# Kernel tuning notes

Hardware: AMD Instinct MI355X
Metric: run time of the kernel (lower is better)

The kernel has to match this reference:

```python
import jax, jax.numpy as jnp
import numpy as np

B, N, E, F, U = 4096, 32, 5, 64, 128

def setup_inputs() -> dict:
    key = jax.random.key(0)
    k1, k2, k3, k4 = jax.random.split(key, 4)
    adjacency = jax.random.uniform(k1, (B, N, N, E), dtype=jnp.float32)
    node = jax.random.normal(k2, (B, N, F), dtype=jnp.float32)
    W1 = jax.random.normal(k3, (E - 1, F, U), dtype=jnp.float32) * (1.0 / np.sqrt(F))
    b1 = jnp.zeros((E - 1, U), dtype=jnp.float32)
    W2 = jax.random.normal(k4, (F, U), dtype=jnp.float32) * (1.0 / np.sqrt(F))
    b2 = jnp.zeros((U,), dtype=jnp.float32)
    return {"adjacency": adjacency, "node": node, "W1": W1, "b1": b1, "W2": W2, "b2": b2}

def reference(adjacency, node, W1, b1, W2, b2):
    # annotations = node (two-input case)
    # Per-edge-type dense projections, stacked on axis 1: [B, E-1, N, U]
    hidden = jnp.einsum('bnf,efu->benu', node, W1) + b1[None, :, None, :]
    # adj: drop edge type 0, transpose to [B, E-1, N, N]
    adj = jnp.transpose(adjacency[:, :, :, 1:], (0, 3, 1, 2))
    # Batched adjacency matmul: [B, E-1, N, N] @ [B, E-1, N, U] -> [B, E-1, N, U]
    msg = jnp.matmul(adj, hidden)
    # Sum over edge types + self-loop dense on node features
    out = jnp.sum(msg, axis=1) + (node @ W2 + b2)
    out = jnp.tanh(out)
    # dropout_rate = 0.0 -> identity
    return (adjacency, node, out)
```

## Files before the change

### kernel.cpp

```cpp
#include <hip/hip_runtime.h>
#include <math.h>

#define Bq 4096
#define Nq 32
#define Eq 5
#define Fq 64
#define Uq 128

constexpr int ADJ_ELEMS  = Bq * Nq * Nq * Eq;
constexpr int NODE_ELEMS = Bq * Nq * Fq;
constexpr int OUT_OFF    = ADJ_ELEMS + NODE_ELEMS;
constexpr int ADJ_B  = Nq * Nq * Eq;
constexpr int NODE_B = Nq * Fq;
constexpr int OUT_B  = Nq * Uq;
constexpr int KTOT = 320;
constexpr int GPAD = 328;
constexpr int NKQ  = KTOT / 32;
constexpr int NNQ  = Uq / 16;
constexpr int WF_ELEMS = NKQ * NNQ * 64 * 8;

typedef __attribute__((ext_vector_type(8))) short bf16x8;
typedef __attribute__((ext_vector_type(4))) float f32x4;

__device__ __forceinline__ ushort f2bf(float x) {
    uint u = __float_as_uint(x);
    return (ushort)((u + 0x7FFF + ((u >> 16) & 1)) >> 16);
}
__device__ __forceinline__ float bf2f(ushort h) { return __uint_as_float(((uint)h) << 16); }

__device__ __forceinline__ int a2idx(int i, int c) {
    return i * 128 + (c ^ ((((i) & 7) << 2) | (((i) >> 3) & 3)));
}

__global__ void wfrag_kernel(const float* __restrict__ W1, const float* __restrict__ W2,
                             ushort* __restrict__ wfH, ushort* __restrict__ wfL) {
    const int tid = blockIdx.x * 256 + threadIdx.x;
    if (tid >= WF_ELEMS) return;
    const int k = tid >> 7;
    const int u = tid & 127;
    const float w = (k < 256) ? W1[k * Uq + u] : W2[(k - 256) * Uq + u];
    const ushort h = f2bf(w);
    const ushort lo = f2bf(w - bf2f(h));
    const int kq = k >> 5, rem = k & 31;
    const int lane = ((rem >> 3) << 4) | (u & 15);
    const int nq = u >> 4;
    const int e = rem & 7;
    const int slot = (((kq * NNQ + nq) * 64 + lane) << 3) + e;
    wfH[slot] = h;
    wfL[slot] = lo;
}

__global__ __launch_bounds__(256, 3) void gcn_kernel(
    const float* __restrict__ adj, const float* __restrict__ node,
    const float* __restrict__ b1, const float* __restrict__ b2,
    const ushort* __restrict__ wfH, const ushort* __restrict__ wfL,
    float* __restrict__ out)
{
    __shared__ uint4 smem4[41984 / 16];
    float*  A2f      = (float*)smem4;
    float*  node_lds = A2f + Nq * 128;
    ushort* Gh       = (ushort*)smem4;
    ushort* Gl       = Gh + Nq * GPAD;
    __shared__ float rowsum[Nq][4];

    const int b = blockIdx.x;
    const int t = threadIdx.x;

    const float* adj_b   = adj + (size_t)b * ADJ_B;
    float*       out_adj = out + (size_t)b * ADJ_B;
    #pragma unroll
    for (int it = 0; it < 5; ++it) {
        const int fi = (t + it * 256) * 4;
        float4 v = *(const float4*)(adj_b + fi);
        *(float4*)(out_adj + fi) = v;
        float vals[4] = {v.x, v.y, v.z, v.w};
        #pragma unroll
        for (int r = 0; r < 4; ++r) {
            const int idx = fi + r;
            const int e  = idx % 5;
            const int ij = idx / 5;
            if (e > 0) {
                const int i = ij >> 5, j = ij & 31;
                A2f[a2idx(i, j * 4 + (e - 1))] = vals[r];
            }
        }
    }

    const float* node_b   = node + (size_t)b * NODE_B;
    float*       out_node = out + ADJ_ELEMS + (size_t)b * NODE_B;
    float nv[8];
    #pragma unroll
    for (int it = 0; it < 2; ++it) {
        const int fi = (t + it * 256) * 4;
        float4 v = *(const float4*)(node_b + fi);
        *(float4*)(out_node + fi) = v;
        *(float4*)(node_lds + fi) = v;
        nv[it * 4 + 0] = v.x; nv[it * 4 + 1] = v.y; nv[it * 4 + 2] = v.z; nv[it * 4 + 3] = v.w;
    }
    __syncthreads();

    float acc[32];
    {
        const int i  = t & 31;
        const int k0 = (t >> 5) * 32;
        const int e  = k0 >> 6;
        const int f0 = k0 & 63;
        #pragma unroll
        for (int kk = 0; kk < 32; ++kk) acc[kk] = 0.f;
        #pragma unroll 4
        for (int j = 0; j < 32; ++j) {
            const float a = A2f[a2idx(i, j * 4 + e)];
            const float4* nrow = (const float4*)(node_lds + j * Fq + f0);
            #pragma unroll
            for (int q = 0; q < 8; ++q) {
                float4 n = nrow[q];
                acc[q*4+0] = fmaf(a, n.x, acc[q*4+0]);
                acc[q*4+1] = fmaf(a, n.y, acc[q*4+1]);
                acc[q*4+2] = fmaf(a, n.z, acc[q*4+2]);
                acc[q*4+3] = fmaf(a, n.w, acc[q*4+3]);
            }
        }
    }
    if (t < 128) {
        const int i = t >> 2, e = t & 3;
        float s = 0.f;
        #pragma unroll 4
        for (int j = 0; j < 32; ++j) s += A2f[a2idx(i, j * 4 + e)];
        rowsum[i][e] = s;
    }
    __syncthreads();

    {
        const int i  = t & 31;
        const int k0 = (t >> 5) * 32;
        #pragma unroll
        for (int kk = 0; kk < 32; kk += 2) {
            const ushort hA = f2bf(acc[kk]);
            const ushort hB = f2bf(acc[kk + 1]);
            const ushort lA = f2bf(acc[kk]     - bf2f(hA));
            const ushort lB = f2bf(acc[kk + 1] - bf2f(hB));
            *(uint*)(Gh + i * GPAD + k0 + kk) = (uint)hA | ((uint)hB << 16);
            *(uint*)(Gl + i * GPAD + k0 + kk) = (uint)lA | ((uint)lB << 16);
        }
        #pragma unroll
        for (int it = 0; it < 2; ++it) {
            const int fi = (t + it * 256) * 4;
            const int ni = fi >> 6, f = fi & 63;
            #pragma unroll
            for (int r = 0; r < 4; r += 2) {
                const ushort hA = f2bf(nv[it*4 + r]);
                const ushort hB = f2bf(nv[it*4 + r + 1]);
                const ushort lA = f2bf(nv[it*4 + r]     - bf2f(hA));
                const ushort lB = f2bf(nv[it*4 + r + 1] - bf2f(hB));
                *(uint*)(Gh + ni * GPAD + 256 + f + r) = (uint)hA | ((uint)hB << 16);
                *(uint*)(Gl + ni * GPAD + 256 + f + r) = (uint)lA | ((uint)lB << 16);
            }
        }
    }
    __syncthreads();

    const int w   = t >> 6;
    const int l   = t & 63;
    const int r16 = l & 15;
    const int khi = l >> 4;
    const int nq0 = w * 2, nq1 = nq0 + 1;

    f32x4 acc00 = {0.f,0.f,0.f,0.f}, acc01 = {0.f,0.f,0.f,0.f};
    f32x4 acc10 = {0.f,0.f,0.f,0.f}, acc11 = {0.f,0.f,0.f,0.f};

    #pragma unroll 2
    for (int kq = 0; kq < NKQ; ++kq) {
        const int kcol = kq * 32 + khi * 8;
        const bf16x8 aH0 = *(const bf16x8*)(Gh + r16        * GPAD + kcol);
        const bf16x8 aH1 = *(const bf16x8*)(Gh + (16 + r16) * GPAD + kcol);
        const bf16x8 aL0 = *(const bf16x8*)(Gl + r16        * GPAD + kcol);
        const bf16x8 aL1 = *(const bf16x8*)(Gl + (16 + r16) * GPAD + kcol);
        const bf16x8 bH0 = *(const bf16x8*)(wfH + (((kq * NNQ + nq0) * 64 + l) << 3));
        const bf16x8 bH1 = *(const bf16x8*)(wfH + (((kq * NNQ + nq1) * 64 + l) << 3));
        const bf16x8 bL0 = *(const bf16x8*)(wfL + (((kq * NNQ + nq0) * 64 + l) << 3));
        const bf16x8 bL1 = *(const bf16x8*)(wfL + (((kq * NNQ + nq1) * 64 + l) << 3));

        acc00 = __builtin_amdgcn_mfma_f32_16x16x32_bf16(aH0, bH0, acc00, 0, 0, 0);
        acc00 = __builtin_amdgcn_mfma_f32_16x16x32_bf16(aH0, bL0, acc00, 0, 0, 0);
        acc00 = __builtin_amdgcn_mfma_f32_16x16x32_bf16(aL0, bH0, acc00, 0, 0, 0);

        acc01 = __builtin_amdgcn_mfma_f32_16x16x32_bf16(aH0, bH1, acc01, 0, 0, 0);
        acc01 = __builtin_amdgcn_mfma_f32_16x16x32_bf16(aH0, bL1, acc01, 0, 0, 0);
        acc01 = __builtin_amdgcn_mfma_f32_16x16x32_bf16(aL0, bH1, acc01, 0, 0, 0);

        acc10 = __builtin_amdgcn_mfma_f32_16x16x32_bf16(aH1, bH0, acc10, 0, 0, 0);
        acc10 = __builtin_amdgcn_mfma_f32_16x16x32_bf16(aH1, bL0, acc10, 0, 0, 0);
        acc10 = __builtin_amdgcn_mfma_f32_16x16x32_bf16(aL1, bH0, acc10, 0, 0, 0);

        acc11 = __builtin_amdgcn_mfma_f32_16x16x32_bf16(aH1, bH1, acc11, 0, 0, 0);
        acc11 = __builtin_amdgcn_mfma_f32_16x16x32_bf16(aH1, bL1, acc11, 0, 0, 0);
        acc11 = __builtin_amdgcn_mfma_f32_16x16x32_bf16(aL1, bH1, acc11, 0, 0, 0);
    }

    float* out_b = out + OUT_OFF + (size_t)b * OUT_B;
    #pragma unroll
    for (int mh = 0; mh < 2; ++mh) {
        #pragma unroll
        for (int nqi = 0; nqi < 2; ++nqi) {
            const f32x4 a = (mh == 0) ? (nqi == 0 ? acc00 : acc01)
                                      : (nqi == 0 ? acc10 : acc11);
            const int u = (w * 2 + nqi) * 16 + r16;
            const float b2u = b2[u];
            const float b1u0 = b1[0 * Uq + u], b1u1 = b1[1 * Uq + u];
            const float b1u2 = b1[2 * Uq + u], b1u3 = b1[3 * Uq + u];
            #pragma unroll
            for (int r = 0; r < 4; ++r) {
                const int i = mh * 16 + khi * 4 + r;
                float pre = a[r] + b2u
                          + rowsum[i][0] * b1u0 + rowsum[i][1] * b1u1
                          + rowsum[i][2] * b1u2 + rowsum[i][3] * b1u3;
                out_b[i * Uq + u] = tanhf(pre);
            }
        }
    }
}

extern "C" void kernel_launch(void* const* d_in, const int* in_sizes, int n_in,
                              void* d_out, int out_size, void* d_ws, size_t ws_size,
                              hipStream_t stream) {
    const float* adj  = (const float*)d_in[0];
    const float* node = (const float*)d_in[1];
    const float* W1   = (const float*)d_in[2];
    const float* b1   = (const float*)d_in[3];
    const float* W2   = (const float*)d_in[4];
    const float* b2   = (const float*)d_in[5];
    float* out = (float*)d_out;

    ushort* wfH = (ushort*)d_ws;
    ushort* wfL = wfH + WF_ELEMS;

    hipLaunchKernelGGL(wfrag_kernel, dim3((WF_ELEMS + 255) / 256), dim3(256), 0, stream,
                       W1, W2, wfH, wfL);
    hipLaunchKernelGGL(gcn_kernel, dim3(Bq), dim3(256), 0, stream,
                       adj, node, b1, b2, wfH, wfL, out);
}
```

Baseline: 357.2 us.

## Compute adjacency-node product and rowsums with split-bf16 MFMA, fast tanh

Replaces the scalar FMA loop that computes adj^T·node per edge type with split-bf16 (hi/lo) MFMA instructions. Adjacency and node values are converted to bf16 fragments directly in LDS, and the row sums are computed with an MFMA against a ones vector. The LDS layout is reorganised with an XOR-swizzled G buffer, and the node self-term block is stored separately. tanhf is replaced by an exp/rcp formulation, which trades some accuracy and adds more conversion work during the load phase.

```diff
diff --git a/kernel.cpp b/kernel.cpp
--- a/kernel.cpp
+++ b/kernel.cpp
@@ -13,14 +13,23 @@
 constexpr int ADJ_B  = Nq * Nq * Eq;
 constexpr int NODE_B = Nq * Fq;
 constexpr int OUT_B  = Nq * Uq;
-constexpr int KTOT = 320;
-constexpr int GPAD = 328;
-constexpr int NKQ  = KTOT / 32;
-constexpr int NNQ  = Uq / 16;
+constexpr int NKQ = 10;
+constexpr int NNQ = Uq / 16;
 constexpr int WF_ELEMS = NKQ * NNQ * 64 * 8;
 
 typedef __attribute__((ext_vector_type(8))) short bf16x8;
 typedef __attribute__((ext_vector_type(4))) float f32x4;
+
+constexpr int GHM_O  = 0;
+constexpr int GLM_O  = 8192;
+constexpr int ADJH_O = 0;
+constexpr int ADJL_O = 4096;
+constexpr int NDH_O  = 8192;
+constexpr int NDL_O  = 10240;
+constexpr int GHS_O  = 16384;
+constexpr int GLS_O  = 18688;
+constexpr int RS_O   = 20992;
+constexpr int SMEM_USH = 21248;
 
 __device__ __forceinline__ ushort f2bf(float x) {
     uint u = __float_as_uint(x);
@@ -28,9 +37,7 @@
 }
 __device__ __forceinline__ float bf2f(ushort h) { return __uint_as_float(((uint)h) << 16); }
 
-__device__ __forceinline__ int a2idx(int i, int c) {
-    return i * 128 + (c ^ ((((i) & 7) << 2) | (((i) >> 3) & 3)));
-}
+#define MFMA(a, b, c) __builtin_amdgcn_mfma_f32_16x16x32_bf16((a), (b), (c), 0, 0, 0)
 
 __global__ void wfrag_kernel(const float* __restrict__ W1, const float* __restrict__ W2,
                              ushort* __restrict__ wfH, ushort* __restrict__ wfL) {
@@ -39,7 +46,7 @@
     const int k = tid >> 7;
     const int u = tid & 127;
     const float w = (k < 256) ? W1[k * Uq + u] : W2[(k - 256) * Uq + u];
-    const ushort h = f2bf(w);
+    const ushort h  = f2bf(w);
     const ushort lo = f2bf(w - bf2f(h));
     const int kq = k >> 5, rem = k & 31;
     const int lane = ((rem >> 3) << 4) | (u & 15);
@@ -56,15 +63,13 @@
     const ushort* __restrict__ wfH, const ushort* __restrict__ wfL,
     float* __restrict__ out)
 {
-    __shared__ uint4 smem4[41984 / 16];
-    float*  A2f      = (float*)smem4;
-    float*  node_lds = A2f + Nq * 128;
-    ushort* Gh       = (ushort*)smem4;
-    ushort* Gl       = Gh + Nq * GPAD;
-    __shared__ float rowsum[Nq][4];
+    __shared__ uint4 smem4[SMEM_USH / 8];
+    ushort* sm = (ushort*)smem4;
+    float* rowsumF = (float*)(sm + RS_O);
 
     const int b = blockIdx.x;
     const int t = threadIdx.x;
+    const int l = t & 63, wv = t >> 6, g = l >> 4, l15 = l & 15;
 
     const float* adj_b   = adj + (size_t)b * ADJ_B;
     float*       out_adj = out + (size_t)b * ADJ_B;
@@ -81,140 +86,179 @@
             const int ij = idx / 5;
             if (e > 0) {
                 const int i = ij >> 5, j = ij & 31;
-                A2f[a2idx(i, j * 4 + (e - 1))] = vals[r];
+                const int slot = ((e - 1) * 2 + (i >> 4)) * 512
+                               + ((((j >> 3) << 4) | (i & 15)) << 3) + (j & 7);
+                const float x = vals[r];
+                const ushort h  = f2bf(x);
+                const ushort lo = f2bf(x - bf2f(h));
+                sm[ADJH_O + slot] = h;
+                sm[ADJL_O + slot] = lo;
             }
         }
     }
 
     const float* node_b   = node + (size_t)b * NODE_B;
     float*       out_node = out + ADJ_ELEMS + (size_t)b * NODE_B;
-    float nv[8];
     #pragma unroll
     for (int it = 0; it < 2; ++it) {
         const int fi = (t + it * 256) * 4;
         float4 v = *(const float4*)(node_b + fi);
         *(float4*)(out_node + fi) = v;
-        *(float4*)(node_lds + fi) = v;
-        nv[it * 4 + 0] = v.x; nv[it * 4 + 1] = v.y; nv[it * 4 + 2] = v.z; nv[it * 4 + 3] = v.w;
+        const int j = fi >> 6, f0 = fi & 63;
+        float vals[4] = {v.x, v.y, v.z, v.w};
+        ushort hs[4], ls[4];
+        #pragma unroll
+        for (int r = 0; r < 4; ++r) {
+            const int f = f0 + r;
+            const float x = vals[r];
+            const ushort h  = f2bf(x);
+            const ushort lo = f2bf(x - bf2f(h));
+            hs[r] = h; ls[r] = lo;
+            const int slotA = (f >> 4) * 512 + ((((j >> 3) << 4) | (f & 15)) << 3) + (j & 7);
+            sm[NDH_O + slotA] = h;
+            sm[NDL_O + slotA] = lo;
+        }
+        uint2 ph, pl;
+        ph.x = (uint)hs[0] | ((uint)hs[1] << 16);
+        ph.y = (uint)hs[2] | ((uint)hs[3] << 16);
+        pl.x = (uint)ls[0] | ((uint)ls[1] << 16);
+        pl.y = (uint)ls[2] | ((uint)ls[3] << 16);
+        *(uint2*)(sm + GHS_O + j * 72 + f0) = ph;
+        *(uint2*)(sm + GLS_O + j * 72 + f0) = pl;
     }
     __syncthreads();
 
-    float acc[32];
+    const int e = wv;
+    f32x4 c1t[4][2];
+    f32x4 rs2[2];
+    #pragma unroll
+    for (int fm = 0; fm < 4; ++fm)
+        #pragma unroll
+        for (int mi = 0; mi < 2; ++mi) c1t[fm][mi] = (f32x4){0.f, 0.f, 0.f, 0.f};
+    rs2[0] = (f32x4){0.f, 0.f, 0.f, 0.f};
+    rs2[1] = (f32x4){0.f, 0.f, 0.f, 0.f};
     {
-        const int i  = t & 31;
-        const int k0 = (t >> 5) * 32;
-        const int e  = k0 >> 6;
-        const int f0 = k0 & 63;
-        #pragma unroll
-        for (int kk = 0; kk < 32; ++kk) acc[kk] = 0.f;
-        #pragma unroll 4
-        for (int j = 0; j < 32; ++j) {
-            const float a = A2f[a2idx(i, j * 4 + e)];
-            const float4* nrow = (const float4*)(node_lds + j * Fq + f0);
-            #pragma unroll
-            for (int q = 0; q < 8; ++q) {
-                float4 n = nrow[q];
-                acc[q*4+0] = fmaf(a, n.x, acc[q*4+0]);
-                acc[q*4+1] = fmaf(a, n.y, acc[q*4+1]);
-                acc[q*4+2] = fmaf(a, n.z, acc[q*4+2]);
-                acc[q*4+3] = fmaf(a, n.w, acc[q*4+3]);
-            }
-        }
-    }
-    if (t < 128) {
-        const int i = t >> 2, e = t & 3;
-        float s = 0.f;
-        #pragma unroll 4
-        for (int j = 0; j < 32; ++j) s += A2f[a2idx(i, j * 4 + e)];
-        rowsum[i][e] = s;
+        bf16x8 nAH[4], nAL[4], bAH[2], bAL[2], onesA;
+        #pragma unroll
+        for (int q = 0; q < 8; ++q) onesA[q] = (short)0x3F80;
+        #pragma unroll
+        for (int fm = 0; fm < 4; ++fm) {
+            nAH[fm] = *(const bf16x8*)(sm + NDH_O + fm * 512 + l * 8);
+            nAL[fm] = *(const bf16x8*)(sm + NDL_O + fm * 512 + l * 8);
+        }
+        #pragma unroll
+        for (int mi = 0; mi < 2; ++mi) {
+            bAH[mi] = *(const bf16x8*)(sm + ADJH_O + (e * 2 + mi) * 512 + l * 8);
+            bAL[mi] = *(const bf16x8*)(sm + ADJL_O + (e * 2 + mi) * 512 + l * 8);
+        }
+        #pragma unroll
+        for (int fm = 0; fm < 4; ++fm)
+            #pragma unroll
+            for (int mi = 0; mi < 2; ++mi) {
+                c1t[fm][mi] = MFMA(nAH[fm], bAH[mi], c1t[fm][mi]);
+                c1t[fm][mi] = MFMA(nAH[fm], bAL[mi], c1t[fm][mi]);
+                c1t[fm][mi] = MFMA(nAL[fm], bAH[mi], c1t[fm][mi]);
+            }
+        #pragma unroll
+        for (int mi = 0; mi < 2; ++mi) {
+            rs2[mi] = MFMA(onesA, bAH[mi], rs2[mi]);
+            rs2[mi] = MFMA(onesA, bAL[mi], rs2[mi]);
+        }
     }
     __syncthreads();
 
-    {
-        const int i  = t & 31;
-        const int k0 = (t >> 5) * 32;
-        #pragma unroll
-        for (int kk = 0; kk < 32; kk += 2) {
-            const ushort hA = f2bf(acc[kk]);
-            const ushort hB = f2bf(acc[kk + 1]);
-            const ushort lA = f2bf(acc[kk]     - bf2f(hA));
-            const ushort lB = f2bf(acc[kk + 1] - bf2f(hB));
-            *(uint*)(Gh + i * GPAD + k0 + kk) = (uint)hA | ((uint)hB << 16);
-            *(uint*)(Gl + i * GPAD + k0 + kk) = (uint)lA | ((uint)lB << 16);
-        }
-        #pragma unroll
-        for (int it = 0; it < 2; ++it) {
-            const int fi = (t + it * 256) * 4;
-            const int ni = fi >> 6, f = fi & 63;
-            #pragma unroll
-            for (int r = 0; r < 4; r += 2) {
-                const ushort hA = f2bf(nv[it*4 + r]);
-                const ushort hB = f2bf(nv[it*4 + r + 1]);
-                const ushort lA = f2bf(nv[it*4 + r]     - bf2f(hA));
-                const ushort lB = f2bf(nv[it*4 + r + 1] - bf2f(hB));
-                *(uint*)(Gh + ni * GPAD + 256 + f + r) = (uint)hA | ((uint)hB << 16);
-                *(uint*)(Gl + ni * GPAD + 256 + f + r) = (uint)lA | ((uint)lB << 16);
-            }
-        }
+    #pragma unroll
+    for (int fm = 0; fm < 4; ++fm) {
+        #pragma unroll
+        for (int mi = 0; mi < 2; ++mi) {
+            const int row = mi * 16 + l15;
+            const int kb  = e * 64 + fm * 16 + g * 4;
+            const int chunk = kb >> 3;
+            const int ush = row * 256 + (((chunk ^ (row & 7)) << 3) | ((kb & 4)));
+            ushort h4[4], l4[4];
+            #pragma unroll
+            for (int r = 0; r < 4; ++r) {
+                const float x = c1t[fm][mi][r];
+                h4[r] = f2bf(x);
+                l4[r] = f2bf(x - bf2f(h4[r]));
+            }
+            uint2 ph, pl;
+            ph.x = (uint)h4[0] | ((uint)h4[1] << 16);
+            ph.y = (uint)h4[2] | ((uint)h4[3] << 16);
+            pl.x = (uint)l4[0] | ((uint)l4[1] << 16);
+            pl.y = (uint)l4[2] | ((uint)l4[3] << 16);
+            *(uint2*)(sm + GHM_O + ush) = ph;
+            *(uint2*)(sm + GLM_O + ush) = pl;
+        }
+    }
+    if (g == 0) {
+        #pragma unroll
+        for (int mi = 0; mi < 2; ++mi)
+            rowsumF[(mi * 16 + l15) * 4 + e] = rs2[mi][0];
     }
     __syncthreads();
 
-    const int w   = t >> 6;
-    const int l   = t & 63;
-    const int r16 = l & 15;
-    const int khi = l >> 4;
-    const int nq0 = w * 2, nq1 = nq0 + 1;
-
-    f32x4 acc00 = {0.f,0.f,0.f,0.f}, acc01 = {0.f,0.f,0.f,0.f};
-    f32x4 acc10 = {0.f,0.f,0.f,0.f}, acc11 = {0.f,0.f,0.f,0.f};
-
-    #pragma unroll 2
-    for (int kq = 0; kq < NKQ; ++kq) {
-        const int kcol = kq * 32 + khi * 8;
-        const bf16x8 aH0 = *(const bf16x8*)(Gh + r16        * GPAD + kcol);
-        const bf16x8 aH1 = *(const bf16x8*)(Gh + (16 + r16) * GPAD + kcol);
-        const bf16x8 aL0 = *(const bf16x8*)(Gl + r16        * GPAD + kcol);
-        const bf16x8 aL1 = *(const bf16x8*)(Gl + (16 + r16) * GPAD + kcol);
-        const bf16x8 bH0 = *(const bf16x8*)(wfH + (((kq * NNQ + nq0) * 64 + l) << 3));
-        const bf16x8 bH1 = *(const bf16x8*)(wfH + (((kq * NNQ + nq1) * 64 + l) << 3));
-        const bf16x8 bL0 = *(const bf16x8*)(wfL + (((kq * NNQ + nq0) * 64 + l) << 3));
-        const bf16x8 bL1 = *(const bf16x8*)(wfL + (((kq * NNQ + nq1) * 64 + l) << 3));
-
-        acc00 = __builtin_amdgcn_mfma_f32_16x16x32_bf16(aH0, bH0, acc00, 0, 0, 0);
-        acc00 = __builtin_amdgcn_mfma_f32_16x16x32_bf16(aH0, bL0, acc00, 0, 0, 0);
-        acc00 = __builtin_amdgcn_mfma_f32_16x16x32_bf16(aL0, bH0, acc00, 0, 0, 0);
-
-        acc01 = __builtin_amdgcn_mfma_f32_16x16x32_bf16(aH0, bH1, acc01, 0, 0, 0);
-        acc01 = __builtin_amdgcn_mfma_f32_16x16x32_bf16(aH0, bL1, acc01, 0, 0, 0);
-        acc01 = __builtin_amdgcn_mfma_f32_16x16x32_bf16(aL0, bH1, acc01, 0, 0, 0);
-
-        acc10 = __builtin_amdgcn_mfma_f32_16x16x32_bf16(aH1, bH0, acc10, 0, 0, 0);
-        acc10 = __builtin_amdgcn_mfma_f32_16x16x32_bf16(aH1, bL0, acc10, 0, 0, 0);
-        acc10 = __builtin_amdgcn_mfma_f32_16x16x32_bf16(aL1, bH0, acc10, 0, 0, 0);
-
-        acc11 = __builtin_amdgcn_mfma_f32_16x16x32_bf16(aH1, bH1, acc11, 0, 0, 0);
-        acc11 = __builtin_amdgcn_mfma_f32_16x16x32_bf16(aH1, bL1, acc11, 0, 0, 0);
-        acc11 = __builtin_amdgcn_mfma_f32_16x16x32_bf16(aL1, bH1, acc11, 0, 0, 0);
+    const int nq0 = wv * 2, nq1 = nq0 + 1;
+    f32x4 acc[2][2];
+    #pragma unroll
+    for (int mi = 0; mi < 2; ++mi)
+        #pragma unroll
+        for (int n = 0; n < 2; ++n) acc[mi][n] = (f32x4){0.f, 0.f, 0.f, 0.f};
+
+    #pragma unroll
+    for (int kq = 0; kq < 10; ++kq) {
+        bf16x8 a2H[2], a2L[2];
+        if (kq < 8) {
+            #pragma unroll
+            for (int mi = 0; mi < 2; ++mi) {
+                const int row = mi * 16 + l15;
+                const int ush = row * 256 + (((kq * 4 + g) ^ (row & 7)) << 3);
+                a2H[mi] = *(const bf16x8*)(sm + GHM_O + ush);
+                a2L[mi] = *(const bf16x8*)(sm + GLM_O + ush);
+            }
+        } else {
+            const int ksl = kq - 8;
+            #pragma unroll
+            for (int mi = 0; mi < 2; ++mi) {
+                const int row = mi * 16 + l15;
+                const int ush = row * 72 + ksl * 32 + g * 8;
+                a2H[mi] = *(const bf16x8*)(sm + GHS_O + ush);
+                a2L[mi] = *(const bf16x8*)(sm + GLS_O + ush);
+            }
+        }
+        const bf16x8 wH0 = *(const bf16x8*)(wfH + ((kq * 8 + nq0) * 64 + l) * 8);
+        const bf16x8 wH1 = *(const bf16x8*)(wfH + ((kq * 8 + nq1) * 64 + l) * 8);
+        const bf16x8 wL0 = *(const bf16x8*)(wfL + ((kq * 8 + nq0) * 64 + l) * 8);
+        const bf16x8 wL1 = *(const bf16x8*)(wfL + ((kq * 8 + nq1) * 64 + l) * 8);
+        #pragma unroll
+        for (int mi = 0; mi < 2; ++mi) {
+            acc[mi][0] = MFMA(a2H[mi], wH0, acc[mi][0]);
+            acc[mi][0] = MFMA(a2H[mi], wL0, acc[mi][0]);
+            acc[mi][0] = MFMA(a2L[mi], wH0, acc[mi][0]);
+            acc[mi][1] = MFMA(a2H[mi], wH1, acc[mi][1]);
+            acc[mi][1] = MFMA(a2H[mi], wL1, acc[mi][1]);
+            acc[mi][1] = MFMA(a2L[mi], wH1, acc[mi][1]);
+        }
     }
 
     float* out_b = out + OUT_OFF + (size_t)b * OUT_B;
     #pragma unroll
-    for (int mh = 0; mh < 2; ++mh) {
+    for (int mi = 0; mi < 2; ++mi) {
         #pragma unroll
         for (int nqi = 0; nqi < 2; ++nqi) {
-            const f32x4 a = (mh == 0) ? (nqi == 0 ? acc00 : acc01)
-                                      : (nqi == 0 ? acc10 : acc11);
-            const int u = (w * 2 + nqi) * 16 + r16;
+            const f32x4 a = acc[mi][nqi];
+            const int u = (wv * 2 + nqi) * 16 + l15;
             const float b2u = b2[u];
-            const float b1u0 = b1[0 * Uq + u], b1u1 = b1[1 * Uq + u];
-            const float b1u2 = b1[2 * Uq + u], b1u3 = b1[3 * Uq + u];
+            const float b10 = b1[0 * Uq + u], b11 = b1[1 * Uq + u];
+            const float b12 = b1[2 * Uq + u], b13 = b1[3 * Uq + u];
             #pragma unroll
             for (int r = 0; r < 4; ++r) {
-                const int i = mh * 16 + khi * 4 + r;
-                float pre = a[r] + b2u
-                          + rowsum[i][0] * b1u0 + rowsum[i][1] * b1u1
-                          + rowsum[i][2] * b1u2 + rowsum[i][3] * b1u3;
-                out_b[i * Uq + u] = tanhf(pre);
+                const int i = mi * 16 + g * 4 + r;
+                const float4 rsv = *(const float4*)(rowsumF + i * 4);
+                float pre = a[r] + b2u + rsv.x * b10 + rsv.y * b11
+                          + rsv.z * b12 + rsv.w * b13;
+                const float ex = __expf(2.0f * pre);
+                out_b[(size_t)i * Uq + u] = 1.0f - 2.0f * __builtin_amdgcn_rcpf(ex + 1.0f);
             }
         }
     }
```

Measured after the change: 316.9 us. 1.13x faster.
